# Optimization experiments

Measured on AMD Instinct MI355X. Metric: run time of the kernel, lower is better.

The kernel has to match this reference:

```python
import jax, jax.numpy as jnp
import numpy as np

N, C, SUBVEC, K, DOUT, DEPTH = 16384, 64, 16, 16, 1024, 4


def setup_inputs() -> dict:
    key = jax.random.key(0)
    k1, k2, k3, k4, k5 = jax.random.split(key, 5)
    x = jax.random.normal(k1, (N, C * SUBVEC), dtype=jnp.float32)
    split_idxs = jax.random.randint(k2, (C, DEPTH), 0, SUBVEC, dtype=jnp.int32)
    split_vals = jax.random.normal(k3, (C, DEPTH, K // 2), dtype=jnp.float32)
    lookup_tables = jax.random.normal(k4, (C, K, DOUT), dtype=jnp.float32)
    bias = jax.random.normal(k5, (DOUT,), dtype=jnp.float32)
    return {"x": x, "split_idxs": split_idxs, "split_vals": split_vals,
            "lookup_tables": lookup_tables, "bias": bias}


def _encode(x_sub, split_idxs, split_vals):
    # x_sub: (n, C, subvec_len); split_idxs: (C, 4); split_vals: (C, 4, 8)
    n = x_sub.shape[0]
    c_idx = jnp.arange(C)
    enc = jnp.zeros((n, C), dtype=jnp.int32)
    for t in range(DEPTH):  # fixed tree depth 4
        xv = x_sub[:, c_idx, split_idxs[:, t]]            # (n, C) selected feature per codebook
        thresh = split_vals[c_idx[None, :], t, enc]       # (n, C) per-node threshold
        enc = 2 * enc + (xv > thresh).astype(jnp.int32)
    return enc  # values in [0, 16)


def reference(x, split_idxs, split_vals, lookup_tables, bias):
    n = x.shape[0]
    x_sub = x.reshape(n, C, SUBVEC)
    enc = _encode(x_sub, split_idxs, split_vals)           # (n, C) int32
    onehot = jax.nn.one_hot(enc, K, dtype=x.dtype)         # (n, C, K)
    out = jnp.einsum('nck,cko->no', onehot, lookup_tables) # sum over codebooks of LUT rows
    return out + bias
```

## Files before the change

kernel.cpp:

```cpp
#include <hip/hip_runtime.h>

#define NN    16384
#define CBN   64
#define SUBV  16
#define KCODE 16
#define DOUTN 1024
#define DEP   4

typedef short bf16x8 __attribute__((ext_vector_type(8)));
typedef float f32x16 __attribute__((ext_vector_type(16)));

static __device__ __forceinline__ unsigned short f2bf(float f) {
  unsigned int u = __float_as_uint(f);
  u += 0x7FFFu + ((u >> 16) & 1u);
  return (unsigned short)(u >> 16);
}

static __device__ __forceinline__ void gld16(const void* g, void* l) {
  __builtin_amdgcn_global_load_lds(
      (const __attribute__((address_space(1))) unsigned int*)g,
      (__attribute__((address_space(3))) unsigned int*)(uintptr_t)l, 16, 0, 0);
}

__global__ __launch_bounds__(256) void prep_k(
    const float* __restrict__ x, const int* __restrict__ split_idxs,
    const float* __restrict__ split_vals, const float* __restrict__ Tg,
    unsigned char* __restrict__ codes, unsigned int* __restrict__ Tswz) {
  const int t = threadIdx.x;

  if (blockIdx.x < 64) {
    const int img = blockIdx.x;
    const int g = img >> 3, ch = img & 7;
    unsigned int* dst = Tswz + (size_t)img * 8192;
    const int colq = t & 31, kp = (t >> 5) & 7;
    #pragma unroll
    for (int cl = 0; cl < 8; ++cl) {
      const float* g0 = Tg + ((size_t)((ch * 8 + cl) * KCODE + 2 * kp)) * DOUTN
                        + g * 128 + colq * 4;
      float4 r0 = *(const float4*)g0;
      float4 r1 = *(const float4*)(g0 + DOUTN);
      unsigned int pk[4] = {
        f2bf(r0.x) | ((unsigned int)f2bf(r1.x) << 16),
        f2bf(r0.y) | ((unsigned int)f2bf(r1.y) << 16),
        f2bf(r0.z) | ((unsigned int)f2bf(r1.z) << 16),
        f2bf(r0.w) | ((unsigned int)f2bf(r1.w) << 16)};
      unsigned key = (unsigned)(colq & 7) << 2;
      #pragma unroll
      for (int j = 0; j < 4; ++j)
        dst[cl * 1024 + ((((unsigned)(colq * 4 + j)) * 8 + (unsigned)kp) ^ key)]
            = pk[j];
    }
    return;
  }

  __shared__ __align__(16) float xs[8][SUBV * CBN];
  __shared__ int   sidxT[DEP * CBN];
  __shared__ float svalT[DEP * (KCODE / 2) * CBN];
  if (t < DEP * CBN) {
    int d = t >> 6, c = t & 63;
    sidxT[t] = split_idxs[c * DEP + d];
  }
  for (int i = t; i < DEP * (KCODE / 2) * CBN; i += 256) {
    int c = i & 63, de = i >> 6, d = de >> 3, e = de & 7;
    svalT[i] = split_vals[(c * DEP + d) * (KCODE / 2) + e];
  }
  const int n0 = (blockIdx.x - 64) * 8;
  const float4* xg = (const float4*)(x + (size_t)n0 * DOUTN);
  #pragma unroll
  for (int i = 0; i < 8; ++i) {
    int li = t + i * 256;
    int r = li >> 8, cpos = li & 255;
    float4 v = xg[r * 256 + cpos];
    int c = cpos >> 2, q = cpos & 3;
    *(float4*)&xs[r][c * SUBV + ((q ^ (c & 3)) << 2)] = v;
  }
  __syncthreads();
  const int c = t & 63, rg = t >> 6;
  #pragma unroll
  for (int i = 0; i < 2; ++i) {
    int nl = rg * 2 + i;
    int e = 0;
    #pragma unroll
    for (int d = 0; d < DEP; ++d) {
      int si = sidxT[d * 64 + c];
      float xv = xs[nl][c * SUBV + (((si >> 2) ^ (c & 3)) << 2) + (si & 3)];
      float th = svalT[(d * 8 + e) * 64 + c];
      e = 2 * e + (xv > th ? 1 : 0);
    }
    codes[(size_t)(n0 + nl) * CBN + c] = (unsigned char)e;
  }
}

__global__ __launch_bounds__(1024, 4) void maddness_mfma(
    const unsigned int* __restrict__ Tswz, const float* __restrict__ bias,
    const unsigned char* __restrict__ codes, float* __restrict__ out) {
  __shared__ __align__(16) unsigned int Tb[32768];

  const int t = threadIdx.x;
  const int wid = t >> 6, lane = t & 63, lrow = lane & 31, h = lane >> 5;
  const int g16 = blockIdx.x, g8 = g16 >> 1, half = g16 & 1;
  const int n0 = blockIdx.y * 1024;
  const char* img = (const char*)Tswz + (size_t)g8 * 8 * 32768;

  #pragma unroll
  for (int i = 0; i < 8; ++i) {
    int gs = wid * 8 + i;
    int ch = gs >> 4, s16 = gs & 15, cl = s16 >> 1, pc = s16 & 1;
    gld16(img + ch * 32768 + cl * 4096 + half * 2048 + pc * 1024 + lane * 16,
          (char*)Tb + gs * 1024);
  }

  const float bv0 = bias[g16 * 64 + lrow];
  const float bv1 = bias[g16 * 64 + 32 + lrow];

  f32x16 acc[2][2];
  #pragma unroll
  for (int rt = 0; rt < 2; ++rt)
    #pragma unroll
    for (int e = 0; e < 16; ++e) { acc[rt][0][e] = bv0; acc[rt][1][e] = bv1; }

  const unsigned char* crow0 = codes + (size_t)(n0 + wid * 64 + lrow) * CBN;
  const unsigned char* crow1 = crow0 + 32 * CBN;
  const unsigned h2 = 2u * (unsigned)h, h2p = h2 + 1u;
  const unsigned rb0 = ((unsigned)lrow * 16 + (unsigned)h * 8)
                     ^ ((((unsigned)lrow >> 2) & 7u) << 3);
  const unsigned cl32 = (unsigned)lrow + 32u;
  const unsigned rb1 = (cl32 * 16 + (unsigned)h * 8)
                     ^ (((cl32 >> 2) & 7u) << 3);

  __syncthreads();

  const int ch0 = wid & 7;
  unsigned long long qA0 = *(const unsigned long long*)(crow0 + ch0 * 8);
  unsigned long long qA1 = *(const unsigned long long*)(crow1 + ch0 * 8);
  const unsigned short* tbc = (const unsigned short*)Tb + ch0 * 8192;
  bf16x8 bP0 = *(const bf16x8*)(tbc + rb0);
  bf16x8 bP1 = *(const bf16x8*)(tbc + rb1);

  #pragma unroll
  for (int i = 0; i < 8; ++i) {
    const int chn = (wid + i + 1) & 7;
    const unsigned short* tbn = (const unsigned short*)Tb + chn * 8192;
    const unsigned long long q0 = qA0, q1 = qA1;
    if (i < 7) {
      qA0 = *(const unsigned long long*)(crow0 + chn * 8);
      qA1 = *(const unsigned long long*)(crow1 + chn * 8);
    }
    #pragma unroll
    for (int cl = 0; cl < 8; ++cl) {
      const bf16x8 b0 = bP0, b1 = bP1;
      if (!(i == 7 && cl == 7)) {
        const unsigned short* tnx = (cl == 7) ? tbn : (tbc + (cl + 1) * 1024);
        bP0 = *(const bf16x8*)(tnx + rb0);
        bP1 = *(const bf16x8*)(tnx + rb1);
      }
      #pragma unroll
      for (int rt = 0; rt < 2; ++rt) {
        const unsigned q32 =
            (unsigned)((rt ? q1 : q0) >> ((cl & 4) ? 32 : 0));
        const unsigned bpos = 8u * (unsigned)(cl & 3);
        const unsigned sh  = (q32 >> bpos) & 3u;
        const unsigned key = (q32 >> (bpos + 2)) & 3u;
        const unsigned long long tt = 0x3F80ULL << (sh << 4);
        union { unsigned long long q[2]; bf16x8 v; } A;
        A.q[0] = (key == h2)  ? tt : 0ULL;
        A.q[1] = (key == h2p) ? tt : 0ULL;
        acc[rt][0] = __builtin_amdgcn_mfma_f32_32x32x16_bf16(A.v, b0, acc[rt][0], 0, 0, 0);
        acc[rt][1] = __builtin_amdgcn_mfma_f32_32x32x16_bf16(A.v, b1, acc[rt][1], 0, 0, 0);
      }
    }
    tbc = tbn;
  }

  #pragma unroll
  for (int ct = 0; ct < 2; ++ct) {
    const int col = g16 * 64 + ct * 32 + lrow;
    #pragma unroll
    for (int rt = 0; rt < 2; ++rt)
      #pragma unroll
      for (int r = 0; r < 16; ++r) {
        int row = n0 + wid * 64 + rt * 32 + (r & 3) + 8 * (r >> 2) + 4 * h;
        out[(size_t)row * DOUTN + col] = acc[rt][ct][r];
      }
  }
}

extern "C" void kernel_launch(void* const* d_in, const int* in_sizes, int n_in,
                              void* d_out, int out_size, void* d_ws, size_t ws_size,
                              hipStream_t stream) {
  const float* x    = (const float*)d_in[0];
  const int*   sidx = (const int*)d_in[1];
  const float* sval = (const float*)d_in[2];
  const float* Tg   = (const float*)d_in[3];
  const float* bias = (const float*)d_in[4];
  float* out = (float*)d_out;
  unsigned char* codes = (unsigned char*)d_ws;
  unsigned int*  Tswz  = (unsigned int*)((char*)d_ws + (1 << 20));

  prep_k<<<64 + NN / 8, 256, 0, stream>>>(x, sidx, sval, Tg, codes, Tswz);
  maddness_mfma<<<dim3(16, 16), 1024, 0, stream>>>(Tswz, bias, codes, out);
}
```

Before: 51.90 us.

## Gather only needed x features in encode and halve MFMA block size

The encode kernel no longer stages full x rows in shared memory. Each thread now gathers just the four split features it needs directly from global memory for four rows, and each block covers 16 rows instead of 8. This reads far less of x, though the gathers are scattered and poorly coalesced. The MFMA kernel moves to 512-thread blocks over 512 rows, so each wave loads one codebook group's LUT slice, and the grid doubles in the row dimension, which raises block count at the cost of reloading the LUT tiles more often.

Result: slower. 56.94 us (+9.7%).

```diff
diff --git a/kernel.cpp b/kernel.cpp
--- a/kernel.cpp
+++ b/kernel.cpp
@@ -53,45 +53,45 @@
     return;
   }
 
-  __shared__ __align__(16) float xs[8][SUBV * CBN];
   __shared__ int   sidxT[DEP * CBN];
   __shared__ float svalT[DEP * (KCODE / 2) * CBN];
   if (t < DEP * CBN) {
     int d = t >> 6, c = t & 63;
     sidxT[t] = split_idxs[c * DEP + d];
   }
-  for (int i = t; i < DEP * (KCODE / 2) * CBN; i += 256) {
-    int c = i & 63, de = i >> 6, d = de >> 3, e = de & 7;
-    svalT[i] = split_vals[(c * DEP + d) * (KCODE / 2) + e];
-  }
-  const int n0 = (blockIdx.x - 64) * 8;
-  const float4* xg = (const float4*)(x + (size_t)n0 * DOUTN);
   #pragma unroll
   for (int i = 0; i < 8; ++i) {
-    int li = t + i * 256;
-    int r = li >> 8, cpos = li & 255;
-    float4 v = xg[r * 256 + cpos];
-    int c = cpos >> 2, q = cpos & 3;
-    *(float4*)&xs[r][c * SUBV + ((q ^ (c & 3)) << 2)] = v;
+    int idx = t + i * 256;
+    int c = idx & 63, de = idx >> 6, d = de >> 3, e = de & 7;
+    svalT[idx] = split_vals[(c * DEP + d) * (KCODE / 2) + e];
   }
   __syncthreads();
+
   const int c = t & 63, rg = t >> 6;
-  #pragma unroll
-  for (int i = 0; i < 2; ++i) {
-    int nl = rg * 2 + i;
+  const size_t r0 = (size_t)(blockIdx.x - 64) * 16 + rg * 4;
+  const float* xr = x + r0 * DOUTN + c * SUBV;
+  const int si0 = sidxT[c],       si1 = sidxT[64 + c],
+            si2 = sidxT[128 + c], si3 = sidxT[192 + c];
+  float xv[4][4];
+  #pragma unroll
+  for (int i = 0; i < 4; ++i) {
+    const float* xri = xr + (size_t)i * DOUTN;
+    xv[i][0] = xri[si0]; xv[i][1] = xri[si1];
+    xv[i][2] = xri[si2]; xv[i][3] = xri[si3];
+  }
+  #pragma unroll
+  for (int i = 0; i < 4; ++i) {
     int e = 0;
     #pragma unroll
     for (int d = 0; d < DEP; ++d) {
-      int si = sidxT[d * 64 + c];
-      float xv = xs[nl][c * SUBV + (((si >> 2) ^ (c & 3)) << 2) + (si & 3)];
       float th = svalT[(d * 8 + e) * 64 + c];
-      e = 2 * e + (xv > th ? 1 : 0);
-    }
-    codes[(size_t)(n0 + nl) * CBN + c] = (unsigned char)e;
-  }
-}
-
-__global__ __launch_bounds__(1024, 4) void maddness_mfma(
+      e = 2 * e + (xv[i][d] > th ? 1 : 0);
+    }
+    codes[(r0 + i) * CBN + c] = (unsigned char)e;
+  }
+}
+
+__global__ __launch_bounds__(512, 2) void maddness_mfma(
     const unsigned int* __restrict__ Tswz, const float* __restrict__ bias,
     const unsigned char* __restrict__ codes, float* __restrict__ out) {
   __shared__ __align__(16) unsigned int Tb[32768];
@@ -99,20 +99,19 @@
   const int t = threadIdx.x;
   const int wid = t >> 6, lane = t & 63, lrow = lane & 31, h = lane >> 5;
   const int g16 = blockIdx.x, g8 = g16 >> 1, half = g16 & 1;
-  const int n0 = blockIdx.y * 1024;
+  const int n0 = blockIdx.y * 512;
   const char* img = (const char*)Tswz + (size_t)g8 * 8 * 32768;
 
   #pragma unroll
-  for (int i = 0; i < 8; ++i) {
-    int gs = wid * 8 + i;
-    int ch = gs >> 4, s16 = gs & 15, cl = s16 >> 1, pc = s16 & 1;
-    gld16(img + ch * 32768 + cl * 4096 + half * 2048 + pc * 1024 + lane * 16,
+  for (int i = 0; i < 16; ++i) {
+    int gs = wid * 16 + i;
+    int cl = i >> 1, pc = i & 1;
+    gld16(img + wid * 32768 + cl * 4096 + half * 2048 + pc * 1024 + lane * 16,
           (char*)Tb + gs * 1024);
   }
 
   const float bv0 = bias[g16 * 64 + lrow];
   const float bv1 = bias[g16 * 64 + 32 + lrow];
-
   f32x16 acc[2][2];
   #pragma unroll
   for (int rt = 0; rt < 2; ++rt)
@@ -130,7 +129,7 @@
 
   __syncthreads();
 
-  const int ch0 = wid & 7;
+  const int ch0 = wid;
   unsigned long long qA0 = *(const unsigned long long*)(crow0 + ch0 * 8);
   unsigned long long qA1 = *(const unsigned long long*)(crow1 + ch0 * 8);
   const unsigned short* tbc = (const unsigned short*)Tb + ch0 * 8192;
@@ -197,6 +196,6 @@
   unsigned char* codes = (unsigned char*)d_ws;
   unsigned int*  Tswz  = (unsigned int*)((char*)d_ws + (1 << 20));
 
-  prep_k<<<64 + NN / 8, 256, 0, stream>>>(x, sidx, sval, Tg, codes, Tswz);
-  maddness_mfma<<<dim3(16, 16), 1024, 0, stream>>>(Tswz, bias, codes, out);
-}
+  prep_k<<<64 + NN / 16, 256, 0, stream>>>(x, sidx, sval, Tg, codes, Tswz);
+  maddness_mfma<<<dim3(16, 32), 512, 0, stream>>>(Tswz, bias, codes, out);
+}
```

## Halve MFMA block size and stage LUT into shared memory in two phases

Applied to the files above, without the earlier changes.

The main kernel now runs 512-thread blocks that each cover 512 rows, with twice as many blocks. The LUT image goes into a 64KB shared buffer in two halves of four codebook groups each, separated by block-wide barriers. This halves shared memory per block so more blocks can sit on a CU, and it doubles the grid to fill more CUs. The cost is that the second staging load is exposed between barriers, and the LUT traffic from global memory doubles across blocks.

Result: slower. 53.68 us (+3.4%).

```diff
diff --git a/kernel.cpp b/kernel.cpp
--- a/kernel.cpp
+++ b/kernel.cpp
@@ -91,28 +91,33 @@
   }
 }
 
-__global__ __launch_bounds__(1024, 4) void maddness_mfma(
+__global__ __launch_bounds__(512, 4) void maddness_mfma(
     const unsigned int* __restrict__ Tswz, const float* __restrict__ bias,
     const unsigned char* __restrict__ codes, float* __restrict__ out) {
-  __shared__ __align__(16) unsigned int Tb[32768];
+  __shared__ __align__(16) unsigned int Tb[16384];
 
   const int t = threadIdx.x;
   const int wid = t >> 6, lane = t & 63, lrow = lane & 31, h = lane >> 5;
   const int g16 = blockIdx.x, g8 = g16 >> 1, half = g16 & 1;
-  const int n0 = blockIdx.y * 1024;
+  const int n0 = blockIdx.y * 512;
   const char* img = (const char*)Tswz + (size_t)g8 * 8 * 32768;
 
-  #pragma unroll
-  for (int i = 0; i < 8; ++i) {
-    int gs = wid * 8 + i;
-    int ch = gs >> 4, s16 = gs & 15, cl = s16 >> 1, pc = s16 & 1;
-    gld16(img + ch * 32768 + cl * 4096 + half * 2048 + pc * 1024 + lane * 16,
-          (char*)Tb + gs * 1024);
-  }
+  #define STAGE(CHBASE)                                                      \
+    {                                                                        \
+      _Pragma("unroll")                                                      \
+      for (int i_ = 0; i_ < 8; ++i_) {                                       \
+        int gs = wid * 8 + i_;                                               \
+        int slot = gs >> 4, s16 = gs & 15, cl = s16 >> 1, pc = s16 & 1;      \
+        gld16(img + ((CHBASE) + slot) * 32768 + cl * 4096 + half * 2048      \
+                  + pc * 1024 + lane * 16,                                   \
+              (char*)Tb + gs * 1024);                                        \
+      }                                                                      \
+    }
+
+  STAGE(0);
 
   const float bv0 = bias[g16 * 64 + lrow];
   const float bv1 = bias[g16 * 64 + 32 + lrow];
-
   f32x16 acc[2][2];
   #pragma unroll
   for (int rt = 0; rt < 2; ++rt)
@@ -130,46 +135,56 @@
 
   __syncthreads();
 
-  const int ch0 = wid & 7;
-  unsigned long long qA0 = *(const unsigned long long*)(crow0 + ch0 * 8);
-  unsigned long long qA1 = *(const unsigned long long*)(crow1 + ch0 * 8);
-  const unsigned short* tbc = (const unsigned short*)Tb + ch0 * 8192;
-  bf16x8 bP0 = *(const bf16x8*)(tbc + rb0);
-  bf16x8 bP1 = *(const bf16x8*)(tbc + rb1);
-
-  #pragma unroll
-  for (int i = 0; i < 8; ++i) {
-    const int chn = (wid + i + 1) & 7;
-    const unsigned short* tbn = (const unsigned short*)Tb + chn * 8192;
-    const unsigned long long q0 = qA0, q1 = qA1;
-    if (i < 7) {
-      qA0 = *(const unsigned long long*)(crow0 + chn * 8);
-      qA1 = *(const unsigned long long*)(crow1 + chn * 8);
-    }
-    #pragma unroll
-    for (int cl = 0; cl < 8; ++cl) {
-      const bf16x8 b0 = bP0, b1 = bP1;
-      if (!(i == 7 && cl == 7)) {
-        const unsigned short* tnx = (cl == 7) ? tbn : (tbc + (cl + 1) * 1024);
-        bP0 = *(const bf16x8*)(tnx + rb0);
-        bP1 = *(const bf16x8*)(tnx + rb1);
+  #pragma unroll
+  for (int p = 0; p < 2; ++p) {
+    const int chbase = p * 4;
+    const int sl0 = wid & 3;
+    unsigned long long qA0 = *(const unsigned long long*)(crow0 + (chbase + sl0) * 8);
+    unsigned long long qA1 = *(const unsigned long long*)(crow1 + (chbase + sl0) * 8);
+    const unsigned short* tbc = (const unsigned short*)Tb + sl0 * 8192;
+    bf16x8 bP0 = *(const bf16x8*)(tbc + rb0);
+    bf16x8 bP1 = *(const bf16x8*)(tbc + rb1);
+
+    #pragma unroll
+    for (int i = 0; i < 4; ++i) {
+      const int sln = (wid + i + 1) & 3;
+      const unsigned short* tbn = (const unsigned short*)Tb + sln * 8192;
+      const unsigned long long q0 = qA0, q1 = qA1;
+      if (i < 3) {
+        qA0 = *(const unsigned long long*)(crow0 + (chbase + sln) * 8);
+        qA1 = *(const unsigned long long*)(crow1 + (chbase + sln) * 8);
       }
       #pragma unroll
-      for (int rt = 0; rt < 2; ++rt) {
-        const unsigned q32 =
-            (unsigned)((rt ? q1 : q0) >> ((cl & 4) ? 32 : 0));
-        const unsigned bpos = 8u * (unsigned)(cl & 3);
-        const unsigned sh  = (q32 >> bpos) & 3u;
-        const unsigned key = (q32 >> (bpos + 2)) & 3u;
-        const unsigned long long tt = 0x3F80ULL << (sh << 4);
-        union { unsigned long long q[2]; bf16x8 v; } A;
-        A.q[0] = (key == h2)  ? tt : 0ULL;
-        A.q[1] = (key == h2p) ? tt : 0ULL;
-        acc[rt][0] = __builtin_amdgcn_mfma_f32_32x32x16_bf16(A.v, b0, acc[rt][0], 0, 0, 0);
-        acc[rt][1] = __builtin_amdgcn_mfma_f32_32x32x16_bf16(A.v, b1, acc[rt][1], 0, 0, 0);
+      for (int cl = 0; cl < 8; ++cl) {
+        const bf16x8 b0 = bP0, b1 = bP1;
+        if (!(i == 3 && cl == 7)) {
+          const unsigned short* tnx = (cl == 7) ? tbn : (tbc + (cl + 1) * 1024);
+          bP0 = *(const bf16x8*)(tnx + rb0);
+          bP1 = *(const bf16x8*)(tnx + rb1);
+        }
+        #pragma unroll
+        for (int rt = 0; rt < 2; ++rt) {
+          const unsigned q32 =
+              (unsigned)((rt ? q1 : q0) >> ((cl & 4) ? 32 : 0));
+          const unsigned bpos = 8u * (unsigned)(cl & 3);
+          const unsigned sh  = (q32 >> bpos) & 3u;
+          const unsigned key = (q32 >> (bpos + 2)) & 3u;
+          const unsigned long long tt = 0x3F80ULL << (sh << 4);
+          union { unsigned long long q[2]; bf16x8 v; } A;
+          A.q[0] = (key == h2)  ? tt : 0ULL;
+          A.q[1] = (key == h2p) ? tt : 0ULL;
+          acc[rt][0] = __builtin_amdgcn_mfma_f32_32x32x16_bf16(A.v, b0, acc[rt][0], 0, 0, 0);
+          acc[rt][1] = __builtin_amdgcn_mfma_f32_32x32x16_bf16(A.v, b1, acc[rt][1], 0, 0, 0);
+        }
       }
-    }
-    tbc = tbn;
+      tbc = tbn;
+    }
+
+    if (p == 0) {
+      __syncthreads();
+      STAGE(4);
+      __syncthreads();
+    }
   }
 
   #pragma unroll
@@ -198,5 +213,5 @@
   unsigned int*  Tswz  = (unsigned int*)((char*)d_ws + (1 << 20));
 
   prep_k<<<64 + NN / 8, 256, 0, stream>>>(x, sidx, sval, Tg, codes, Tswz);
-  maddness_mfma<<<dim3(16, 16), 1024, 0, stream>>>(Tswz, bias, codes, out);
-}
+  maddness_mfma<<<dim3(16, 32), 512, 0, stream>>>(Tswz, bias, codes, out);
+}
```
